# Kernel optimization log

Hardware: AMD Instinct MI355X
Metric: run time of the kernel (lower is better)

Reference implementation:

```python
import jax, jax.numpy as jnp
import numpy as np

N, E, B = 20000, 640000, 4096
IN_DIM, HID, A, D, C = 128, 256, 8, 64, 2


def setup_inputs() -> dict:
    key = jax.random.key(0)
    ks = jax.random.split(key, 16)
    inp = {
        "feature": jax.random.normal(ks[0], (N, IN_DIM), dtype=jnp.float32),
        "src": jax.random.randint(ks[1], (E,), 0, N),
        "dst": jax.random.randint(ks[2], (E,), 0, N),
        "pairs": jax.random.randint(ks[3], (B, 2), 0, N),
        # gcn1.linear: in_dim -> hid
        "W1": jax.random.normal(ks[4], (HID, IN_DIM), dtype=jnp.float32) * 0.02,
        "b1": jnp.zeros((HID,), dtype=jnp.float32),
        # aspEmbed (no bias): hid -> A*D
        "aspW": jax.random.normal(ks[5], (A * D, HID), dtype=jnp.float32) * 0.02,
        # Aspect_Representation.linear: D -> 1
        "attW": jax.random.normal(ks[6], (1, D), dtype=jnp.float32) * 0.02,
        "attb": jnp.zeros((1,), dtype=jnp.float32),
        # aspect_merge_linear: D -> 1
        "mergeW": jax.random.normal(ks[7], (1, D), dtype=jnp.float32) * 0.02,
        "mergeb": jnp.zeros((1,), dtype=jnp.float32),
        # concat_linear: 2A -> C
        "catW": jax.random.normal(ks[8], (C, 2 * A), dtype=jnp.float32) * 0.02,
        "catb": jnp.zeros((C,), dtype=jnp.float32),
    }
    return inp


def _aspect_head(pe, aspW, attW, attb, mergeW, mergeb):
    # pe: [B, HID]
    b = pe.shape[0]
    asp = (pe @ aspW.T).reshape(b, A, D)               # [B, A, D]
    score = jax.nn.softmax(asp @ attW.T + attb, axis=1)  # [B, A, 1] softmax over aspects
    rep = score * asp                                   # [B, A, D]
    return (rep @ mergeW.T + mergeb)[..., 0]            # [B, A]


def reference(feature, src, dst, pairs, W1, b1, aspW, attW, attb,
              mergeW, mergeb, catW, catb):
    n = feature.shape[0]
    nf = feature + feature.mean(axis=0)                 # node_feature
    # GCNLayer: u_mul_v message + mean aggregation at dst
    msg = nf[src] * nf[dst]                             # [E, IN_DIM]
    agg = jax.ops.segment_sum(msg, dst, num_segments=n)
    deg = jax.ops.segment_sum(jnp.ones((msg.shape[0],), dtype=feature.dtype), dst, num_segments=n)
    x = agg / jnp.where(deg > 0, deg, 1.0)[:, None]
    x = x @ W1.T + b1                                   # [N, HID] (dropout = identity in eval)
    p1 = _aspect_head(x[pairs[:, 0]], aspW, attW, attb, mergeW, mergeb)
    p2 = _aspect_head(x[pairs[:, 1]], aspW, attW, attb, mergeW, mergeb)
    out = jnp.concatenate([p1, p2], axis=1) @ catW.T + catb  # [B, C]
    return jax.nn.log_softmax(out, axis=-1)
```

## Files before the change

### kernel.cpp

```cpp
#include <hip/hip_runtime.h>
#include <hip/hip_bf16.h>

constexpr int IN_DIM = 128;
constexpr int HID    = 256;
constexpr int A_     = 8;
constexpr int D_     = 64;
constexpr int PAD    = 128;
constexpr int CS_ROWS = 32;

__global__ void k1_prep_zero(const float* __restrict__ aspW, const float* __restrict__ attW,
                             const float* __restrict__ mergeW, const float* __restrict__ b1,
                             const float* __restrict__ attb, const float* __restrict__ W1,
                             float* __restrict__ WS, float* __restrict__ WM,
                             float* __restrict__ sb, float* __restrict__ mb,
                             ulonglong2* __restrict__ zbase, int n16) {
  if (blockIdx.x >= A_) {
    int i = (blockIdx.x - A_) * blockDim.x + threadIdx.x;
    int stride = (gridDim.x - A_) * blockDim.x;
    ulonglong2 z; z.x = 0ull; z.y = 0ull;
    for (; i < n16; i += stride) zbase[i] = z;
    return;
  }
  __shared__ float Us[HID], Um[HID];
  __shared__ float r1[HID], r2[HID];
  int a = blockIdx.x;
  int h = threadIdx.x;
  float ss = 0.f, sm = 0.f;
  const float* ap = aspW + (size_t)(a * D_) * HID + h;
#pragma unroll 8
  for (int d = 0; d < D_; ++d) {
    float w = ap[(size_t)d * HID];
    ss += attW[d] * w;
    sm += mergeW[d] * w;
  }
  Us[h] = ss;
  Um[h] = sm;
  float bv = b1[h];
  r1[h] = ss * bv;
  r2[h] = sm * bv;
  __syncthreads();
  for (int ofs = HID / 2; ofs > 0; ofs >>= 1) {
    if (h < ofs) { r1[h] += r1[h + ofs]; r2[h] += r2[h + ofs]; }
    __syncthreads();
  }
  if (h == 0) { sb[a] = r1[0] + attb[0]; mb[a] = r2[0]; }
  __syncthreads();
  int j = h & 127, half = h >> 7;
  float ws = 0.f, wm = 0.f;
  const float* w1p = W1 + (size_t)(half * 128) * IN_DIM + j;
  const float* usp = Us + half * 128;
  const float* ump = Um + half * 128;
#pragma unroll 16
  for (int k = 0; k < 128; ++k) {
    float w = w1p[(size_t)k * IN_DIM];
    ws += usp[k] * w;
    wm += ump[k] * w;
  }
  r1[h] = ws;
  r2[h] = wm;
  __syncthreads();
  if (h < IN_DIM) {
    WS[a * IN_DIM + h] = r1[h] + r1[h + 128];
    WM[a * IN_DIM + h] = r2[h] + r2[h + 128];
  }
}

__global__ void k2_colsum_mask(const float* __restrict__ f, float* __restrict__ pb, int N,
                               int npart, const int* __restrict__ pairs,
                               int* __restrict__ mask, int* __restrict__ wl,
                               int* __restrict__ wlcnt, int nIdx) {
  if ((int)blockIdx.x >= npart) {
    int i = ((int)blockIdx.x - npart) * blockDim.x + threadIdx.x;
    if (i < nIdx) {
      int node = pairs[i];
      if (atomicCAS(&mask[node], 0, 1) == 0) {
        int p = atomicAdd(wlcnt, 1);
        wl[p] = node;
      }
    }
    return;
  }
  __shared__ float sm[8][IN_DIM];
  int tid = threadIdx.x;
  int c4  = tid & 31;
  int r   = tid >> 5;
  int base = blockIdx.x * CS_ROWS;
  float4 acc = make_float4(0.f, 0.f, 0.f, 0.f);
#pragma unroll
  for (int it = 0; it < CS_ROWS / 8; ++it) {
    int row = base + it * 8 + r;
    if (row < N) {
      float4 v = ((const float4*)f)[(size_t)row * 32 + c4];
      acc.x += v.x; acc.y += v.y; acc.z += v.z; acc.w += v.w;
    }
  }
  ((float4*)sm[r])[c4] = acc;
  __syncthreads();
  if (tid < IN_DIM) {
    float s = 0.f;
#pragma unroll
    for (int rr = 0; rr < 8; ++rr) s += sm[rr][tid];
    pb[(size_t)blockIdx.x * IN_DIM + tid] = s;
  }
}

__global__ void k3_fill_colred(const int4* __restrict__ src4, const int4* __restrict__ dst4,
                               const int* __restrict__ mask, int* __restrict__ cnt,
                               int* __restrict__ esrc, int E4, int fillBlocks,
                               const float* __restrict__ pb, float* __restrict__ colsum,
                               int npart) {
  if ((int)blockIdx.x >= fillBlocks) {
    int rblk = (int)blockIdx.x - fillBlocks;
    int t = threadIdx.x;
    float4 acc = make_float4(0.f, 0.f, 0.f, 0.f);
    for (int row = t; row < npart; row += 256) {
      float4 v = ((const float4*)(pb + (size_t)row * IN_DIM))[rblk];
      acc.x += v.x; acc.y += v.y; acc.z += v.z; acc.w += v.w;
    }
    __shared__ float4 red[256];
    red[t] = acc;
    __syncthreads();
    for (int ofs = 128; ofs > 0; ofs >>= 1) {
      if (t < ofs) {
        float4 o = red[t + ofs];
        red[t].x += o.x; red[t].y += o.y; red[t].z += o.z; red[t].w += o.w;
      }
      __syncthreads();
    }
    if (t == 0) ((float4*)colsum)[rblk] = red[0];
    return;
  }
  int e = blockIdx.x * blockDim.x + threadIdx.x;
  if (e >= E4) return;
  int4 d = dst4[e];
  int4 s = src4[e];
  if (mask[d.x]) { int p = atomicAdd(&cnt[d.x], 1); if (p < PAD) esrc[(size_t)d.x * PAD + p] = s.x; }
  if (mask[d.y]) { int p = atomicAdd(&cnt[d.y], 1); if (p < PAD) esrc[(size_t)d.y * PAD + p] = s.y; }
  if (mask[d.z]) { int p = atomicAdd(&cnt[d.z], 1); if (p < PAD) esrc[(size_t)d.z * PAD + p] = s.z; }
  if (mask[d.w]) { int p = atomicAdd(&cnt[d.w], 1); if (p < PAD) esrc[(size_t)d.w * PAD + p] = s.w; }
}

__global__ void __launch_bounds__(64) pull_k(
    const float* __restrict__ feat, const float* __restrict__ colsum,
    const int* __restrict__ cnt, const int* __restrict__ esrc,
    const int* __restrict__ wl, const int* __restrict__ wlcnt,
    const float* __restrict__ WS, const float* __restrict__ WM,
    float* __restrict__ nodevals, float invN) {
  int widx = blockIdx.x;
  if (widx >= *wlcnt) return;
  int d = wl[widx];
  int lane = threadIdx.x;
  int deg = cnt[d];
  const float2* F = (const float2*)feat;
  const int* es = esrc + (size_t)d * PAD;
  int n = deg < PAD ? deg : PAD;
  float2 acc = make_float2(0.f, 0.f);
  int i = 0;
  for (; i + 7 < n; i += 8) {
    float2 v0 = F[(size_t)es[i + 0] * 64 + lane];
    float2 v1 = F[(size_t)es[i + 1] * 64 + lane];
    float2 v2 = F[(size_t)es[i + 2] * 64 + lane];
    float2 v3 = F[(size_t)es[i + 3] * 64 + lane];
    float2 v4 = F[(size_t)es[i + 4] * 64 + lane];
    float2 v5 = F[(size_t)es[i + 5] * 64 + lane];
    float2 v6 = F[(size_t)es[i + 6] * 64 + lane];
    float2 v7 = F[(size_t)es[i + 7] * 64 + lane];
    acc.x += ((v0.x + v1.x) + (v2.x + v3.x)) + ((v4.x + v5.x) + (v6.x + v7.x));
    acc.y += ((v0.y + v1.y) + (v2.y + v3.y)) + ((v4.y + v5.y) + (v6.y + v7.y));
  }
  for (; i < n; ++i) {
    float2 v0 = F[(size_t)es[i] * 64 + lane];
    acc.x += v0.x;
    acc.y += v0.y;
  }
  float2 cm = ((const float2*)colsum)[lane];
  cm.x *= invN;
  cm.y *= invN;
  float2 fd = F[(size_t)d * 64 + lane];
  float2 x;
  if (deg > 0) {
    float inv = 1.0f / (float)deg;
    x.x = (fd.x + cm.x) * (acc.x * inv + cm.x);
    x.y = (fd.y + cm.y) * (acc.y * inv + cm.y);
  } else {
    x.x = 0.f;
    x.y = 0.f;
  }
  float v[16];
#pragma unroll
  for (int a = 0; a < A_; ++a) {
    float2 w = ((const float2*)WS)[a * 64 + lane];
    float2 u = ((const float2*)WM)[a * 64 + lane];
    v[a] = x.x * w.x + x.y * w.y;
    v[8 + a] = x.x * u.x + x.y * u.y;
  }
#pragma unroll
  for (int m = 32; m > 0; m >>= 1) {
#pragma unroll
    for (int k = 0; k < 16; ++k) v[k] += __shfl_xor(v[k], m, 64);
  }
  if (lane == 0) {
#pragma unroll
    for (int k = 0; k < 16; ++k) nodevals[(size_t)d * 16 + k] = v[k];
  }
}

__global__ void pair_k(const int* __restrict__ pairs, const float* __restrict__ nodevals,
                       const float* __restrict__ sb, const float* __restrict__ mb,
                       const float* __restrict__ catW, const float* __restrict__ catb,
                       const float* __restrict__ mergeb, float* __restrict__ out, int B) {
  int b = blockIdx.x * blockDim.x + threadIdx.x;
  if (b >= B) return;
  float mgb = mergeb[0];
  float p[2 * A_];
  for (int side = 0; side < 2; ++side) {
    int node = pairs[b * 2 + side];
    const float4* nv = (const float4*)(nodevals + (size_t)node * 16);
    float4 q0 = nv[0], q1 = nv[1], q2 = nv[2], q3 = nv[3];
    float s[A_] = {q0.x, q0.y, q0.z, q0.w, q1.x, q1.y, q1.z, q1.w};
    float m[A_] = {q2.x, q2.y, q2.z, q2.w, q3.x, q3.y, q3.z, q3.w};
#pragma unroll
    for (int a = 0; a < A_; ++a) { s[a] += sb[a]; m[a] += mb[a]; }
    float mx = s[0];
#pragma unroll
    for (int a = 1; a < A_; ++a) mx = fmaxf(mx, s[a]);
    float es[A_], sum = 0.f;
#pragma unroll
    for (int a = 0; a < A_; ++a) { es[a] = __expf(s[a] - mx); sum += es[a]; }
    float rsum = 1.0f / sum;
#pragma unroll
    for (int a = 0; a < A_; ++a) p[side * A_ + a] = es[a] * rsum * m[a] + mgb;
  }
  float o0 = catb[0], o1 = catb[1];
#pragma unroll
  for (int k = 0; k < 2 * A_; ++k) {
    o0 += p[k] * catW[k];
    o1 += p[k] * catW[2 * A_ + k];
  }
  float mx = fmaxf(o0, o1);
  float lse = mx + logf(__expf(o0 - mx) + __expf(o1 - mx));
  out[b * 2 + 0] = o0 - lse;
  out[b * 2 + 1] = o1 - lse;
}

extern "C" void kernel_launch(void* const* d_in, const int* in_sizes, int n_in,
                              void* d_out, int out_size, void* d_ws, size_t ws_size,
                              hipStream_t stream) {
  const float* feature = (const float*)d_in[0];
  const int*   src     = (const int*)d_in[1];
  const int*   dst     = (const int*)d_in[2];
  const int*   pairs   = (const int*)d_in[3];
  const float* W1      = (const float*)d_in[4];
  const float* b1      = (const float*)d_in[5];
  const float* aspW    = (const float*)d_in[6];
  const float* attW    = (const float*)d_in[7];
  const float* attb    = (const float*)d_in[8];
  const float* mergeW  = (const float*)d_in[9];
  const float* mergebp = (const float*)d_in[10];
  const float* catW    = (const float*)d_in[11];
  const float* catb    = (const float*)d_in[12];

  const int N = in_sizes[0] / IN_DIM;
  const int E = in_sizes[1];
  const int B = in_sizes[3] / 2;
  const int npart = (N + CS_ROWS - 1) / CS_ROWS;
  const int maskBlocks = (2 * B + 255) / 256;
  const int fillBlocks = (E / 4 + 255) / 256;
  const int E4 = E / 4;

  char* ws = (char*)d_ws;
  size_t off_b = 0;
  int* cnt = (int*)(ws + off_b);        off_b += (size_t)N * sizeof(int);
  int* mask = (int*)(ws + off_b);       off_b += (size_t)N * sizeof(int);
  int* wlcnt = (int*)(ws + off_b);      off_b += 4 * sizeof(int);
  size_t zero_bytes = (off_b + 15) & ~(size_t)15;
  off_b = zero_bytes;
  float* colsum = (float*)(ws + off_b); off_b += IN_DIM * sizeof(float);
  float* pb = (float*)(ws + off_b);     off_b += (size_t)npart * IN_DIM * sizeof(float);
  int* wl = (int*)(ws + off_b);         off_b += (size_t)(2 * B) * sizeof(int);
  float* WS = (float*)(ws + off_b);     off_b += A_ * IN_DIM * sizeof(float);
  float* WM = (float*)(ws + off_b);     off_b += A_ * IN_DIM * sizeof(float);
  float* sb = (float*)(ws + off_b);     off_b += A_ * sizeof(float);
  float* mb = (float*)(ws + off_b);     off_b += A_ * sizeof(float);
  float* nodevals = (float*)(ws + off_b); off_b += (size_t)N * 16 * sizeof(float);
  int* esrc = (int*)(ws + off_b);       off_b += (size_t)N * PAD * sizeof(int);

  k1_prep_zero<<<A_ + 40, 256, 0, stream>>>(aspW, attW, mergeW, b1, attb, W1,
                                            WS, WM, sb, mb,
                                            (ulonglong2*)d_ws, (int)(zero_bytes / 16));
  k2_colsum_mask<<<npart + maskBlocks, 256, 0, stream>>>(feature, pb, N, npart,
                                                         pairs, mask, wl, wlcnt, 2 * B);
  k3_fill_colred<<<fillBlocks + 32, 256, 0, stream>>>((const int4*)src, (const int4*)dst,
                                                      mask, cnt, esrc, E4, fillBlocks,
                                                      pb, colsum, npart);
  pull_k<<<2 * B, 64, 0, stream>>>(feature, colsum, cnt, esrc, wl, wlcnt, WS, WM,
                                   nodevals, 1.0f / (float)N);
  pair_k<<<(B + 255) / 256, 256, 0, stream>>>(pairs, nodevals, sb, mb, catW, catb,
                                              mergebp, (float*)d_out, B);
}
```

Measured before the change: 57.22 us.

## Fuse colsum into prep kernel and drop pair-node dedup mask and worklist

Folds the feature column-sum partials into the first prep/zeroing kernel, which removes the separate mask/worklist kernel and one launch. The edge fill now records sources for every destination node instead of only the nodes used by pairs. The pull kernel runs once per pair slot and writes results indexed by slot, so the pair kernel reads them directly. The trade-off is roughly three times more atomics and scattered esrc writes in the fill, plus duplicate pull work for repeated pair nodes, in exchange for fewer kernels and no dedup atomics. CS_ROWS is halved, which gives more colsum blocks.

Result: slower. 72.24 us (+26.2%).

```diff
diff --git a/kernel.cpp b/kernel.cpp
--- a/kernel.cpp
+++ b/kernel.cpp
@@ -6,24 +6,52 @@
 constexpr int A_     = 8;
 constexpr int D_     = 64;
 constexpr int PAD    = 128;
-constexpr int CS_ROWS = 32;
-
-__global__ void k1_prep_zero(const float* __restrict__ aspW, const float* __restrict__ attW,
-                             const float* __restrict__ mergeW, const float* __restrict__ b1,
-                             const float* __restrict__ attb, const float* __restrict__ W1,
-                             float* __restrict__ WS, float* __restrict__ WM,
-                             float* __restrict__ sb, float* __restrict__ mb,
-                             ulonglong2* __restrict__ zbase, int n16) {
-  if (blockIdx.x >= A_) {
-    int i = (blockIdx.x - A_) * blockDim.x + threadIdx.x;
-    int stride = (gridDim.x - A_) * blockDim.x;
+constexpr int CS_ROWS = 16;
+
+__global__ void k1_prep_zero_colsum(const float* __restrict__ aspW, const float* __restrict__ attW,
+                                    const float* __restrict__ mergeW, const float* __restrict__ b1,
+                                    const float* __restrict__ attb, const float* __restrict__ W1,
+                                    float* __restrict__ WS, float* __restrict__ WM,
+                                    float* __restrict__ sb, float* __restrict__ mb,
+                                    ulonglong2* __restrict__ zbase, int n16,
+                                    const float* __restrict__ feat, float* __restrict__ pb,
+                                    int N) {
+  int bid = blockIdx.x;
+  if (bid >= 16) {
+    __shared__ float sm[8][IN_DIM];
+    int tid = threadIdx.x;
+    int c4  = tid & 31;
+    int r   = tid >> 5;
+    int base = (bid - 16) * CS_ROWS;
+    float4 acc = make_float4(0.f, 0.f, 0.f, 0.f);
+#pragma unroll
+    for (int it = 0; it < CS_ROWS / 8; ++it) {
+      int row = base + it * 8 + r;
+      if (row < N) {
+        float4 v = ((const float4*)feat)[(size_t)row * 32 + c4];
+        acc.x += v.x; acc.y += v.y; acc.z += v.z; acc.w += v.w;
+      }
+    }
+    ((float4*)sm[r])[c4] = acc;
+    __syncthreads();
+    if (tid < IN_DIM) {
+      float s = 0.f;
+#pragma unroll
+      for (int rr = 0; rr < 8; ++rr) s += sm[rr][tid];
+      pb[(size_t)(bid - 16) * IN_DIM + tid] = s;
+    }
+    return;
+  }
+  if (bid >= A_) {
+    int i = (bid - A_) * blockDim.x + threadIdx.x;
+    int stride = 8 * blockDim.x;
     ulonglong2 z; z.x = 0ull; z.y = 0ull;
     for (; i < n16; i += stride) zbase[i] = z;
     return;
   }
   __shared__ float Us[HID], Um[HID];
   __shared__ float r1[HID], r2[HID];
-  int a = blockIdx.x;
+  int a = bid;
   int h = threadIdx.x;
   float ss = 0.f, sm = 0.f;
   const float* ap = aspW + (size_t)(a * D_) * HID + h;
@@ -65,50 +93,10 @@
   }
 }
 
-__global__ void k2_colsum_mask(const float* __restrict__ f, float* __restrict__ pb, int N,
-                               int npart, const int* __restrict__ pairs,
-                               int* __restrict__ mask, int* __restrict__ wl,
-                               int* __restrict__ wlcnt, int nIdx) {
-  if ((int)blockIdx.x >= npart) {
-    int i = ((int)blockIdx.x - npart) * blockDim.x + threadIdx.x;
-    if (i < nIdx) {
-      int node = pairs[i];
-      if (atomicCAS(&mask[node], 0, 1) == 0) {
-        int p = atomicAdd(wlcnt, 1);
-        wl[p] = node;
-      }
-    }
-    return;
-  }
-  __shared__ float sm[8][IN_DIM];
-  int tid = threadIdx.x;
-  int c4  = tid & 31;
-  int r   = tid >> 5;
-  int base = blockIdx.x * CS_ROWS;
-  float4 acc = make_float4(0.f, 0.f, 0.f, 0.f);
-#pragma unroll
-  for (int it = 0; it < CS_ROWS / 8; ++it) {
-    int row = base + it * 8 + r;
-    if (row < N) {
-      float4 v = ((const float4*)f)[(size_t)row * 32 + c4];
-      acc.x += v.x; acc.y += v.y; acc.z += v.z; acc.w += v.w;
-    }
-  }
-  ((float4*)sm[r])[c4] = acc;
-  __syncthreads();
-  if (tid < IN_DIM) {
-    float s = 0.f;
-#pragma unroll
-    for (int rr = 0; rr < 8; ++rr) s += sm[rr][tid];
-    pb[(size_t)blockIdx.x * IN_DIM + tid] = s;
-  }
-}
-
-__global__ void k3_fill_colred(const int4* __restrict__ src4, const int4* __restrict__ dst4,
-                               const int* __restrict__ mask, int* __restrict__ cnt,
-                               int* __restrict__ esrc, int E4, int fillBlocks,
-                               const float* __restrict__ pb, float* __restrict__ colsum,
-                               int npart) {
+__global__ void k2_fill_colred(const int4* __restrict__ src4, const int4* __restrict__ dst4,
+                               int* __restrict__ cnt, int* __restrict__ esrc, int E4,
+                               int fillBlocks, const float* __restrict__ pb,
+                               float* __restrict__ colsum, int npart) {
   if ((int)blockIdx.x >= fillBlocks) {
     int rblk = (int)blockIdx.x - fillBlocks;
     int t = threadIdx.x;
@@ -134,21 +122,19 @@
   if (e >= E4) return;
   int4 d = dst4[e];
   int4 s = src4[e];
-  if (mask[d.x]) { int p = atomicAdd(&cnt[d.x], 1); if (p < PAD) esrc[(size_t)d.x * PAD + p] = s.x; }
-  if (mask[d.y]) { int p = atomicAdd(&cnt[d.y], 1); if (p < PAD) esrc[(size_t)d.y * PAD + p] = s.y; }
-  if (mask[d.z]) { int p = atomicAdd(&cnt[d.z], 1); if (p < PAD) esrc[(size_t)d.z * PAD + p] = s.z; }
-  if (mask[d.w]) { int p = atomicAdd(&cnt[d.w], 1); if (p < PAD) esrc[(size_t)d.w * PAD + p] = s.w; }
+  { int p = atomicAdd(&cnt[d.x], 1); if (p < PAD) esrc[(size_t)d.x * PAD + p] = s.x; }
+  { int p = atomicAdd(&cnt[d.y], 1); if (p < PAD) esrc[(size_t)d.y * PAD + p] = s.y; }
+  { int p = atomicAdd(&cnt[d.z], 1); if (p < PAD) esrc[(size_t)d.z * PAD + p] = s.z; }
+  { int p = atomicAdd(&cnt[d.w], 1); if (p < PAD) esrc[(size_t)d.w * PAD + p] = s.w; }
 }
 
 __global__ void __launch_bounds__(64) pull_k(
     const float* __restrict__ feat, const float* __restrict__ colsum,
     const int* __restrict__ cnt, const int* __restrict__ esrc,
-    const int* __restrict__ wl, const int* __restrict__ wlcnt,
-    const float* __restrict__ WS, const float* __restrict__ WM,
-    float* __restrict__ nodevals, float invN) {
-  int widx = blockIdx.x;
-  if (widx >= *wlcnt) return;
-  int d = wl[widx];
+    const int* __restrict__ pairsFlat, const float* __restrict__ WS,
+    const float* __restrict__ WM, float* __restrict__ slotvals, float invN) {
+  int slot = blockIdx.x;
+  int d = pairsFlat[slot];
   int lane = threadIdx.x;
   int deg = cnt[d];
   const float2* F = (const float2*)feat;
@@ -201,11 +187,11 @@
   }
   if (lane == 0) {
 #pragma unroll
-    for (int k = 0; k < 16; ++k) nodevals[(size_t)d * 16 + k] = v[k];
-  }
-}
-
-__global__ void pair_k(const int* __restrict__ pairs, const float* __restrict__ nodevals,
+    for (int k = 0; k < 16; ++k) slotvals[(size_t)slot * 16 + k] = v[k];
+  }
+}
+
+__global__ void pair_k(const float* __restrict__ slotvals,
                        const float* __restrict__ sb, const float* __restrict__ mb,
                        const float* __restrict__ catW, const float* __restrict__ catb,
                        const float* __restrict__ mergeb, float* __restrict__ out, int B) {
@@ -214,8 +200,7 @@
   float mgb = mergeb[0];
   float p[2 * A_];
   for (int side = 0; side < 2; ++side) {
-    int node = pairs[b * 2 + side];
-    const float4* nv = (const float4*)(nodevals + (size_t)node * 16);
+    const float4* nv = (const float4*)(slotvals + (size_t)(2 * b + side) * 16);
     float4 q0 = nv[0], q1 = nv[1], q2 = nv[2], q3 = nv[3];
     float s[A_] = {q0.x, q0.y, q0.z, q0.w, q1.x, q1.y, q1.z, q1.w};
     float m[A_] = {q2.x, q2.y, q2.z, q2.w, q3.x, q3.y, q3.z, q3.w};
@@ -264,37 +249,30 @@
   const int E = in_sizes[1];
   const int B = in_sizes[3] / 2;
   const int npart = (N + CS_ROWS - 1) / CS_ROWS;
-  const int maskBlocks = (2 * B + 255) / 256;
   const int fillBlocks = (E / 4 + 255) / 256;
   const int E4 = E / 4;
 
   char* ws = (char*)d_ws;
   size_t off_b = 0;
   int* cnt = (int*)(ws + off_b);        off_b += (size_t)N * sizeof(int);
-  int* mask = (int*)(ws + off_b);       off_b += (size_t)N * sizeof(int);
-  int* wlcnt = (int*)(ws + off_b);      off_b += 4 * sizeof(int);
   size_t zero_bytes = (off_b + 15) & ~(size_t)15;
   off_b = zero_bytes;
   float* colsum = (float*)(ws + off_b); off_b += IN_DIM * sizeof(float);
   float* pb = (float*)(ws + off_b);     off_b += (size_t)npart * IN_DIM * sizeof(float);
-  int* wl = (int*)(ws + off_b);         off_b += (size_t)(2 * B) * sizeof(int);
   float* WS = (float*)(ws + off_b);     off_b += A_ * IN_DIM * sizeof(float);
   float* WM = (float*)(ws + off_b);     off_b += A_ * IN_DIM * sizeof(float);
   float* sb = (float*)(ws + off_b);     off_b += A_ * sizeof(float);
   float* mb = (float*)(ws + off_b);     off_b += A_ * sizeof(float);
-  float* nodevals = (float*)(ws + off_b); off_b += (size_t)N * 16 * sizeof(float);
+  float* slotvals = (float*)(ws + off_b); off_b += (size_t)(2 * B) * 16 * sizeof(float);
   int* esrc = (int*)(ws + off_b);       off_b += (size_t)N * PAD * sizeof(int);
 
-  k1_prep_zero<<<A_ + 40, 256, 0, stream>>>(aspW, attW, mergeW, b1, attb, W1,
-                                            WS, WM, sb, mb,
-                                            (ulonglong2*)d_ws, (int)(zero_bytes / 16));
-  k2_colsum_mask<<<npart + maskBlocks, 256, 0, stream>>>(feature, pb, N, npart,
-                                                         pairs, mask, wl, wlcnt, 2 * B);
-  k3_fill_colred<<<fillBlocks + 32, 256, 0, stream>>>((const int4*)src, (const int4*)dst,
-                                                      mask, cnt, esrc, E4, fillBlocks,
-                                                      pb, colsum, npart);
-  pull_k<<<2 * B, 64, 0, stream>>>(feature, colsum, cnt, esrc, wl, wlcnt, WS, WM,
-                                   nodevals, 1.0f / (float)N);
-  pair_k<<<(B + 255) / 256, 256, 0, stream>>>(pairs, nodevals, sb, mb, catW, catb,
+  k1_prep_zero_colsum<<<16 + npart, 256, 0, stream>>>(
+      aspW, attW, mergeW, b1, attb, W1, WS, WM, sb, mb,
+      (ulonglong2*)d_ws, (int)(zero_bytes / 16), feature, pb, N);
+  k2_fill_colred<<<fillBlocks + 32, 256, 0, stream>>>(
+      (const int4*)src, (const int4*)dst, cnt, esrc, E4, fillBlocks, pb, colsum, npart);
+  pull_k<<<2 * B, 64, 0, stream>>>(feature, colsum, cnt, esrc, pairs, WS, WM,
+                                   slotvals, 1.0f / (float)N);
+  pair_k<<<(B + 255) / 256, 256, 0, stream>>>(slotvals, sb, mb, catW, catb,
                                               mergebp, (float*)d_out, B);
 }
```

## Fuse prep, zeroing, colsum and dedup mask into one kernel with bitmask

Applied to the files above, without the earlier changes.

Merges the weight-prep, workspace zeroing, column partial sums and pair-node dedup into one 1024-thread kernel, which removes a launch. The dedup now builds a 20000-bit bitmask in shared memory inside a single block instead of doing CAS on a global int mask, so the N-int mask no longer needs to be zeroed. The edge-fill kernel tests bits from this compact bitmask, which is more cache-friendly. Risks: the single dedup block serialises 8192 atomics, each colsum block reads only one float4 per thread, and the bitmask is fixed at 1024 words, which caps N at 32768.

Result: faster. 49.20 us (median of 2 runs) (-14.0%).

```diff
diff --git a/kernel.cpp b/kernel.cpp
--- a/kernel.cpp
+++ b/kernel.cpp
@@ -6,106 +6,134 @@
 constexpr int A_     = 8;
 constexpr int D_     = 64;
 constexpr int PAD    = 128;
-constexpr int CS_ROWS = 32;
-
-__global__ void k1_prep_zero(const float* __restrict__ aspW, const float* __restrict__ attW,
-                             const float* __restrict__ mergeW, const float* __restrict__ b1,
-                             const float* __restrict__ attb, const float* __restrict__ W1,
-                             float* __restrict__ WS, float* __restrict__ WM,
-                             float* __restrict__ sb, float* __restrict__ mb,
-                             ulonglong2* __restrict__ zbase, int n16) {
-  if (blockIdx.x >= A_) {
-    int i = (blockIdx.x - A_) * blockDim.x + threadIdx.x;
-    int stride = (gridDim.x - A_) * blockDim.x;
+constexpr int NBITW  = 1024;
+
+__global__ __launch_bounds__(1024) void k1_all(
+    const float* __restrict__ aspW, const float* __restrict__ attW,
+    const float* __restrict__ mergeW, const float* __restrict__ b1,
+    const float* __restrict__ attb, const float* __restrict__ W1,
+    const float* __restrict__ feat, const int* __restrict__ pairsFlat,
+    float* __restrict__ WS, float* __restrict__ WM,
+    float* __restrict__ sb, float* __restrict__ mb,
+    unsigned int* __restrict__ bitsG, int* __restrict__ wl, int* __restrict__ wlcnt,
+    ulonglong2* __restrict__ zbase, int n16,
+    float* __restrict__ pb, int N, int nIdx) {
+  __shared__ float smem[4096];
+  const int bid = blockIdx.x;
+  const int t = threadIdx.x;
+
+  if (bid == 0) {
+    unsigned int* bits = (unsigned int*)smem;
+    __shared__ int cnt_l;
+    if (t < NBITW) bits[t] = 0u;
+    if (t == 0) cnt_l = 0;
+    __syncthreads();
+#pragma unroll
+    for (int k = 0; k < 8; ++k) {
+      int i = k * 1024 + t;
+      if (i < nIdx) {
+        int node = pairsFlat[i];
+        unsigned int m = 1u << (node & 31);
+        unsigned int old = atomicOr(&bits[node >> 5], m);
+        if ((old & m) == 0u) {
+          int p = atomicAdd(&cnt_l, 1);
+          wl[p] = node;
+        }
+      }
+    }
+    __syncthreads();
+    if (t < NBITW) bitsG[t] = bits[t];
+    if (t == 0) *wlcnt = cnt_l;
+    return;
+  }
+  if (bid <= A_) {
+    int a = bid - 1;
+    float* psS = smem;
+    float* psM = smem + 1024;
+    float* Us  = smem + 2048;
+    float* Um  = smem + 2304;
+    float* r1  = smem + 2560;
+    float* r2  = smem + 2816;
+    {
+      int h = t & 255, dq = t >> 8;
+      float ss = 0.f, sm = 0.f;
+      const float* ap = aspW + (size_t)(a * D_ + dq * 16) * HID + h;
+#pragma unroll
+      for (int d = 0; d < 16; ++d) {
+        float w = ap[(size_t)d * HID];
+        ss += attW[dq * 16 + d] * w;
+        sm += mergeW[dq * 16 + d] * w;
+      }
+      psS[dq * 256 + h] = ss;
+      psM[dq * 256 + h] = sm;
+    }
+    __syncthreads();
+    if (t < HID) {
+      float us = psS[t] + psS[256 + t] + psS[512 + t] + psS[768 + t];
+      float um = psM[t] + psM[256 + t] + psM[512 + t] + psM[768 + t];
+      Us[t] = us; Um[t] = um;
+      float bv = b1[t];
+      r1[t] = us * bv; r2[t] = um * bv;
+    }
+    __syncthreads();
+    for (int ofs = 128; ofs > 0; ofs >>= 1) {
+      if (t < ofs) { r1[t] += r1[t + ofs]; r2[t] += r2[t + ofs]; }
+      __syncthreads();
+    }
+    if (t == 0) { sb[a] = r1[0] + attb[0]; mb[a] = r2[0]; }
+    __syncthreads();
+    {
+      int j = t & 127, ch = t >> 7;
+      float ws = 0.f, wm = 0.f;
+      const float* w1p = W1 + (size_t)(ch * 32) * IN_DIM + j;
+      const float* usp = Us + ch * 32;
+      const float* ump = Um + ch * 32;
+#pragma unroll
+      for (int k = 0; k < 32; ++k) {
+        float w = w1p[(size_t)k * IN_DIM];
+        ws += usp[k] * w;
+        wm += ump[k] * w;
+      }
+      psS[ch * 128 + j] = ws;
+      psM[ch * 128 + j] = wm;
+    }
+    __syncthreads();
+    if (t < IN_DIM) {
+      float ws = 0.f, wm = 0.f;
+#pragma unroll
+      for (int c = 0; c < 8; ++c) { ws += psS[c * 128 + t]; wm += psM[c * 128 + t]; }
+      WS[a * IN_DIM + t] = ws;
+      WM[a * IN_DIM + t] = wm;
+    }
+    return;
+  }
+  if (bid <= 16) {
     ulonglong2 z; z.x = 0ull; z.y = 0ull;
-    for (; i < n16; i += stride) zbase[i] = z;
+    for (int i = (bid - 9) * 1024 + t; i < n16; i += 8 * 1024) zbase[i] = z;
     return;
   }
-  __shared__ float Us[HID], Um[HID];
-  __shared__ float r1[HID], r2[HID];
-  int a = blockIdx.x;
-  int h = threadIdx.x;
-  float ss = 0.f, sm = 0.f;
-  const float* ap = aspW + (size_t)(a * D_) * HID + h;
+  {
+    int cb = bid - 17;
+    int rslot = t >> 5, c4 = t & 31;
+    int row = cb * 32 + rslot;
+    float4 acc = make_float4(0.f, 0.f, 0.f, 0.f);
+    if (row < N) {
+      float4 v = ((const float4*)feat)[(size_t)row * 32 + c4];
+      acc = v;
+    }
+    ((float4*)smem)[rslot * 32 + c4] = acc;
+    __syncthreads();
+    if (t < IN_DIM) {
+      float s = 0.f;
 #pragma unroll 8
-  for (int d = 0; d < D_; ++d) {
-    float w = ap[(size_t)d * HID];
-    ss += attW[d] * w;
-    sm += mergeW[d] * w;
-  }
-  Us[h] = ss;
-  Um[h] = sm;
-  float bv = b1[h];
-  r1[h] = ss * bv;
-  r2[h] = sm * bv;
-  __syncthreads();
-  for (int ofs = HID / 2; ofs > 0; ofs >>= 1) {
-    if (h < ofs) { r1[h] += r1[h + ofs]; r2[h] += r2[h + ofs]; }
-    __syncthreads();
-  }
-  if (h == 0) { sb[a] = r1[0] + attb[0]; mb[a] = r2[0]; }
-  __syncthreads();
-  int j = h & 127, half = h >> 7;
-  float ws = 0.f, wm = 0.f;
-  const float* w1p = W1 + (size_t)(half * 128) * IN_DIM + j;
-  const float* usp = Us + half * 128;
-  const float* ump = Um + half * 128;
-#pragma unroll 16
-  for (int k = 0; k < 128; ++k) {
-    float w = w1p[(size_t)k * IN_DIM];
-    ws += usp[k] * w;
-    wm += ump[k] * w;
-  }
-  r1[h] = ws;
-  r2[h] = wm;
-  __syncthreads();
-  if (h < IN_DIM) {
-    WS[a * IN_DIM + h] = r1[h] + r1[h + 128];
-    WM[a * IN_DIM + h] = r2[h] + r2[h + 128];
-  }
-}
-
-__global__ void k2_colsum_mask(const float* __restrict__ f, float* __restrict__ pb, int N,
-                               int npart, const int* __restrict__ pairs,
-                               int* __restrict__ mask, int* __restrict__ wl,
-                               int* __restrict__ wlcnt, int nIdx) {
-  if ((int)blockIdx.x >= npart) {
-    int i = ((int)blockIdx.x - npart) * blockDim.x + threadIdx.x;
-    if (i < nIdx) {
-      int node = pairs[i];
-      if (atomicCAS(&mask[node], 0, 1) == 0) {
-        int p = atomicAdd(wlcnt, 1);
-        wl[p] = node;
-      }
-    }
-    return;
-  }
-  __shared__ float sm[8][IN_DIM];
-  int tid = threadIdx.x;
-  int c4  = tid & 31;
-  int r   = tid >> 5;
-  int base = blockIdx.x * CS_ROWS;
-  float4 acc = make_float4(0.f, 0.f, 0.f, 0.f);
-#pragma unroll
-  for (int it = 0; it < CS_ROWS / 8; ++it) {
-    int row = base + it * 8 + r;
-    if (row < N) {
-      float4 v = ((const float4*)f)[(size_t)row * 32 + c4];
-      acc.x += v.x; acc.y += v.y; acc.z += v.z; acc.w += v.w;
-    }
-  }
-  ((float4*)sm[r])[c4] = acc;
-  __syncthreads();
-  if (tid < IN_DIM) {
-    float s = 0.f;
-#pragma unroll
-    for (int rr = 0; rr < 8; ++rr) s += sm[rr][tid];
-    pb[(size_t)blockIdx.x * IN_DIM + tid] = s;
-  }
-}
-
-__global__ void k3_fill_colred(const int4* __restrict__ src4, const int4* __restrict__ dst4,
-                               const int* __restrict__ mask, int* __restrict__ cnt,
+      for (int r = 0; r < 32; ++r) s += smem[r * IN_DIM + t];
+      pb[(size_t)cb * IN_DIM + t] = s;
+    }
+  }
+}
+
+__global__ void k2_fill_colred(const int4* __restrict__ src4, const int4* __restrict__ dst4,
+                               const unsigned int* __restrict__ bitsG, int* __restrict__ cnt,
                                int* __restrict__ esrc, int E4, int fillBlocks,
                                const float* __restrict__ pb, float* __restrict__ colsum,
                                int npart) {
@@ -134,10 +162,10 @@
   if (e >= E4) return;
   int4 d = dst4[e];
   int4 s = src4[e];
-  if (mask[d.x]) { int p = atomicAdd(&cnt[d.x], 1); if (p < PAD) esrc[(size_t)d.x * PAD + p] = s.x; }
-  if (mask[d.y]) { int p = atomicAdd(&cnt[d.y], 1); if (p < PAD) esrc[(size_t)d.y * PAD + p] = s.y; }
-  if (mask[d.z]) { int p = atomicAdd(&cnt[d.z], 1); if (p < PAD) esrc[(size_t)d.z * PAD + p] = s.z; }
-  if (mask[d.w]) { int p = atomicAdd(&cnt[d.w], 1); if (p < PAD) esrc[(size_t)d.w * PAD + p] = s.w; }
+  if ((bitsG[d.x >> 5] >> (d.x & 31)) & 1u) { int p = atomicAdd(&cnt[d.x], 1); if (p < PAD) esrc[(size_t)d.x * PAD + p] = s.x; }
+  if ((bitsG[d.y >> 5] >> (d.y & 31)) & 1u) { int p = atomicAdd(&cnt[d.y], 1); if (p < PAD) esrc[(size_t)d.y * PAD + p] = s.y; }
+  if ((bitsG[d.z >> 5] >> (d.z & 31)) & 1u) { int p = atomicAdd(&cnt[d.z], 1); if (p < PAD) esrc[(size_t)d.z * PAD + p] = s.z; }
+  if ((bitsG[d.w >> 5] >> (d.w & 31)) & 1u) { int p = atomicAdd(&cnt[d.w], 1); if (p < PAD) esrc[(size_t)d.w * PAD + p] = s.w; }
 }
 
 __global__ void __launch_bounds__(64) pull_k(
@@ -263,21 +291,20 @@
   const int N = in_sizes[0] / IN_DIM;
   const int E = in_sizes[1];
   const int B = in_sizes[3] / 2;
-  const int npart = (N + CS_ROWS - 1) / CS_ROWS;
-  const int maskBlocks = (2 * B + 255) / 256;
+  const int npart = (N + 31) / 32;
   const int fillBlocks = (E / 4 + 255) / 256;
   const int E4 = E / 4;
 
   char* ws = (char*)d_ws;
   size_t off_b = 0;
   int* cnt = (int*)(ws + off_b);        off_b += (size_t)N * sizeof(int);
-  int* mask = (int*)(ws + off_b);       off_b += (size_t)N * sizeof(int);
-  int* wlcnt = (int*)(ws + off_b);      off_b += 4 * sizeof(int);
   size_t zero_bytes = (off_b + 15) & ~(size_t)15;
   off_b = zero_bytes;
+  unsigned int* bitsG = (unsigned int*)(ws + off_b); off_b += NBITW * sizeof(unsigned int);
+  int* wlcnt = (int*)(ws + off_b);      off_b += 4 * sizeof(int);
+  int* wl = (int*)(ws + off_b);         off_b += (size_t)(2 * B) * sizeof(int);
   float* colsum = (float*)(ws + off_b); off_b += IN_DIM * sizeof(float);
   float* pb = (float*)(ws + off_b);     off_b += (size_t)npart * IN_DIM * sizeof(float);
-  int* wl = (int*)(ws + off_b);         off_b += (size_t)(2 * B) * sizeof(int);
   float* WS = (float*)(ws + off_b);     off_b += A_ * IN_DIM * sizeof(float);
   float* WM = (float*)(ws + off_b);     off_b += A_ * IN_DIM * sizeof(float);
   float* sb = (float*)(ws + off_b);     off_b += A_ * sizeof(float);
@@ -285,14 +312,13 @@
   float* nodevals = (float*)(ws + off_b); off_b += (size_t)N * 16 * sizeof(float);
   int* esrc = (int*)(ws + off_b);       off_b += (size_t)N * PAD * sizeof(int);
 
-  k1_prep_zero<<<A_ + 40, 256, 0, stream>>>(aspW, attW, mergeW, b1, attb, W1,
-                                            WS, WM, sb, mb,
-                                            (ulonglong2*)d_ws, (int)(zero_bytes / 16));
-  k2_colsum_mask<<<npart + maskBlocks, 256, 0, stream>>>(feature, pb, N, npart,
-                                                         pairs, mask, wl, wlcnt, 2 * B);
-  k3_fill_colred<<<fillBlocks + 32, 256, 0, stream>>>((const int4*)src, (const int4*)dst,
-                                                      mask, cnt, esrc, E4, fillBlocks,
-                                                      pb, colsum, npart);
+  k1_all<<<17 + npart, 1024, 0, stream>>>(
+      aspW, attW, mergeW, b1, attb, W1, feature, pairs,
+      WS, WM, sb, mb, bitsG, wl, wlcnt,
+      (ulonglong2*)d_ws, (int)(zero_bytes / 16), pb, N, 2 * B);
+  k2_fill_colred<<<fillBlocks + 32, 256, 0, stream>>>(
+      (const int4*)src, (const int4*)dst, bitsG, cnt, esrc, E4, fillBlocks,
+      pb, colsum, npart);
   pull_k<<<2 * B, 64, 0, stream>>>(feature, colsum, cnt, esrc, wl, wlcnt, WS, WM,
                                    nodevals, 1.0f / (float)N);
   pair_k<<<(B + 255) / 256, 256, 0, stream>>>(pairs, nodevals, sb, mb, catW, catb,
```
